# Kernel tuning notes

Hardware: AMD Instinct MI355X
Metric: run time of the kernel (lower is better)

The kernel has to match this reference:

```python
import jax, jax.numpy as jnp
import numpy as np

DIM, NUM_HEADS, N_POINTS = 256, 8, 4
N_Q, N_KV = 32768, 32768


def setup_inputs() -> dict:
    key = jax.random.key(0)
    ks = jax.random.split(key, 16)
    C, H, P = DIM, NUM_HEADS, N_POINTS
    s = 1.0 / np.sqrt(C)
    inp = {
        "query": jax.random.normal(ks[0], (N_Q, C), jnp.float32),
        "key": jax.random.normal(ks[1], (N_KV, C), jnp.float32),
        "value": jax.random.normal(ks[2], (N_KV, C), jnp.float32),
        # reference_points: Linear(C, 2*H*P)
        "Wr": jax.random.normal(ks[3], (C, 2 * H * P), jnp.float32) * s,
        "br": jnp.zeros((2 * H * P,), jnp.float32),
        # offset_attn: Linear(C, H*P*2)
        "Wo": jax.random.normal(ks[4], (C, H * P * 2), jnp.float32) * s,
        "bo": jnp.zeros((H * P * 2,), jnp.float32),
        # value_proj: Linear(C, C)
        "Wv": jax.random.normal(ks[5], (C, C), jnp.float32) * s,
        "bv": jnp.zeros((C,), jnp.float32),
        # output_proj: Linear(C, C)
        "Wout": jax.random.normal(ks[6], (C, C), jnp.float32) * s,
        "bout": jnp.zeros((C,), jnp.float32),
    }
    return inp


def reference(query, key, value, Wr, br, Wo, bo, Wv, bv, Wout, bout):
    N, C = query.shape
    M = value.shape[0]
    H, P = NUM_HEADS, N_POINTS
    Ch = C // H

    # sampling locations in [0,1] (ref) plus unconstrained offsets
    ref = jax.nn.sigmoid((query @ Wr + br).reshape(N, H, P, 2))
    off = (query @ Wo + bo).reshape(N, H, P, 2)
    loc = ref + off                              # [N,H,P,2]

    # 1-D bilinear interpolation along the token axis. The original's
    # 4-term (wx,wy) expression algebraically collapses to a pure lerp in x:
    # (1-wx)(1-wy)+ (1-wx)wy = (1-wx), wx(1-wy)+wx*wy = wx.
    x = loc[..., 0] * (M - 1)                    # [N,H,P]
    x0 = jnp.clip(jnp.floor(x).astype(jnp.int32), 0, M - 1)
    x1 = jnp.clip(x0 + 1, 0, M - 1)
    wx = (x - x0.astype(x.dtype))[..., None]     # [N,H,P,1]

    hidx = jnp.arange(H)[None, :, None]          # head-aligned gather index

    def sample(table):                           # table: [M,H,Ch]
        g0 = table[x0, hidx]                     # [N,H,P,Ch]
        g1 = table[x1, hidx]
        return (1.0 - wx) * g0 + wx * g1

    v = (value @ Wv + bv).reshape(M, H, Ch)      # value_proj, split heads
    sv = sample(v)                               # [N,H,P,Ch] sampled values

    # attention weights from query/key: sample per-head keys at the same
    # locations, dot with per-head queries, softmax over the P points
    k = key.reshape(M, H, Ch)
    sk = sample(k)                               # [N,H,P,Ch]
    q = query.reshape(N, H, Ch)
    scores = jnp.einsum("nhc,nhpc->nhp", q, sk) / jnp.sqrt(
        jnp.asarray(Ch, query.dtype)
    )
    attn = jax.nn.softmax(scores, axis=-1)       # [N,H,P]

    out = jnp.einsum("nhp,nhpc->nhc", attn, sv).reshape(N, C)
    return out @ Wout + bout
```

## Files before the change

### kernel.cpp

```cpp
#include <hip/hip_runtime.h>
#include <hip/hip_bf16.h>
#include <stdint.h>

#define NQ    32768
#define NKV   32768
#define CDIM  256
#define NHEADS 8
#define NPTS  4

using bf16x8 = __attribute__((ext_vector_type(8))) short;
using f32x4  = __attribute__((ext_vector_type(4))) float;
using u16x8  = __attribute__((ext_vector_type(8))) ushort;

static __device__ __forceinline__ ushort f2bf(float f) {
  uint32_t u = __float_as_uint(f);
  return (ushort)((u + 0x7FFFu + ((u >> 16) & 1u)) >> 16);
}
static __device__ __forceinline__ float bf2f(ushort h) {
  return __uint_as_float(((uint32_t)h) << 16);
}
static __device__ __forceinline__ void async16(const void* g, void* l) {
  __builtin_amdgcn_global_load_lds(
      (const __attribute__((address_space(1))) uint32_t*)g,
      (__attribute__((address_space(3))) uint32_t*)l, 16, 0, 0);
}
#define WAIT_VM(N) do { asm volatile("s_waitcnt vmcnt(" #N ")" ::: "memory"); \
                        __builtin_amdgcn_sched_barrier(0); } while (0)

__global__ __launch_bounds__(256) void transpose_w(const float* __restrict__ W,
                                                   ushort* __restrict__ WT) {
  int j = blockIdx.x, k = threadIdx.x;
  WT[j * 256 + k] = f2bf(W[k * 256 + j]);
}

__global__ __launch_bounds__(256) void gemm_mfma(
    const ushort* __restrict__ A, const ushort* __restrict__ BT,
    const float* __restrict__ bias, ushort* __restrict__ Cb,
    float* __restrict__ Cf, int out_bf16) {
  __shared__ ushort Alds[128 * 32];
  __shared__ ushort Blds[128 * 32];
  const int t = threadIdx.x;
  const int wave = t >> 6, lane = t & 63;
  const int mt = blockIdx.x >> 1, nt = blockIdx.x & 1;
  const int m0 = mt * 128, n0 = nt * 128;
  const int wr = wave >> 1, wc = wave & 1;
  const int r16 = lane & 15, kb = (lane >> 4) * 8;

  f32x4 acc[4][4] = {};

  for (int kt = 0; kt < 256; kt += 32) {
    __syncthreads();
#pragma unroll
    for (int it = 0; it < 2; ++it) {
      int c = it * 256 + t;
      int row = c >> 2, cc = c & 3;
      async16(A  + ((size_t)(m0 + row) * 256 + kt + cc * 8),
              Alds + (size_t)(it * 256 + wave * 64) * 8);
      async16(BT + ((size_t)(n0 + row) * 256 + kt + cc * 8),
              Blds + (size_t)(it * 256 + wave * 64) * 8);
    }
    __syncthreads();

    bf16x8 af[4], bfr[4];
#pragma unroll
    for (int m = 0; m < 4; ++m)
      af[m] = *(const bf16x8*)&Alds[(wr * 64 + m * 16 + r16) * 32 + kb];
#pragma unroll
    for (int n = 0; n < 4; ++n)
      bfr[n] = *(const bf16x8*)&Blds[(wc * 64 + n * 16 + r16) * 32 + kb];
#pragma unroll
    for (int m = 0; m < 4; ++m)
#pragma unroll
      for (int n = 0; n < 4; ++n)
        acc[m][n] = __builtin_amdgcn_mfma_f32_16x16x32_bf16(af[m], bfr[n],
                                                            acc[m][n], 0, 0, 0);
  }

  const int rg = lane >> 4;
#pragma unroll
  for (int m = 0; m < 4; ++m)
#pragma unroll
    for (int n = 0; n < 4; ++n) {
      int gc = n0 + wc * 64 + n * 16 + r16;
      float bb = bias[gc];
#pragma unroll
      for (int r = 0; r < 4; ++r) {
        int gr = m0 + wr * 64 + m * 16 + rg * 4 + r;
        float v = acc[m][n][r] + bb;
        if (out_bf16) Cb[(size_t)gr * 256 + gc] = f2bf(v);
        else          Cf[(size_t)gr * 256 + gc] = v;
      }
    }
}

__global__ __launch_bounds__(256) void gemm_mfma_fa(
    const float* __restrict__ Af, const ushort* __restrict__ BT,
    const float* __restrict__ bias, ushort* __restrict__ Cb) {
  __shared__ ushort Alds[128 * 32];
  __shared__ ushort Blds[128 * 32];
  const int t = threadIdx.x;
  const int wave = t >> 6, lane = t & 63;
  const int mt = blockIdx.x >> 1, nt = blockIdx.x & 1;
  const int m0 = mt * 128, n0 = nt * 128;
  const int wr = wave >> 1, wc = wave & 1;
  const int r16 = lane & 15, kb = (lane >> 4) * 8;

  f32x4 acc[4][4] = {};

  for (int kt = 0; kt < 256; kt += 32) {
    __syncthreads();
#pragma unroll
    for (int it = 0; it < 2; ++it) {
      int c = it * 256 + t;
      int row = c >> 2, cc = c & 3;
      async16(BT + ((size_t)(n0 + row) * 256 + kt + cc * 8),
              Blds + (size_t)(it * 256 + wave * 64) * 8);
    }
#pragma unroll
    for (int it = 0; it < 2; ++it) {
      int c = it * 256 + t;
      int row = c >> 2, cc = c & 3;
      const float* src = Af + (size_t)(m0 + row) * 256 + kt + cc * 8;
      f32x4 a = *(const f32x4*)src;
      f32x4 b = *(const f32x4*)(src + 4);
      u16x8 w;
#pragma unroll
      for (int e = 0; e < 4; ++e) { w[e] = f2bf(a[e]); w[4 + e] = f2bf(b[e]); }
      *(u16x8*)&Alds[(size_t)c * 8] = w;
    }
    __syncthreads();

    bf16x8 af[4], bfr[4];
#pragma unroll
    for (int m = 0; m < 4; ++m)
      af[m] = *(const bf16x8*)&Alds[(wr * 64 + m * 16 + r16) * 32 + kb];
#pragma unroll
    for (int n = 0; n < 4; ++n)
      bfr[n] = *(const bf16x8*)&Blds[(wc * 64 + n * 16 + r16) * 32 + kb];
#pragma unroll
    for (int m = 0; m < 4; ++m)
#pragma unroll
      for (int n = 0; n < 4; ++n)
        acc[m][n] = __builtin_amdgcn_mfma_f32_16x16x32_bf16(af[m], bfr[n],
                                                            acc[m][n], 0, 0, 0);
  }

  const int rg = lane >> 4;
#pragma unroll
  for (int m = 0; m < 4; ++m)
#pragma unroll
    for (int n = 0; n < 4; ++n) {
      int gc = n0 + wc * 64 + n * 16 + r16;
      float bb = bias[gc];
#pragma unroll
      for (int r = 0; r < 4; ++r) {
        int gr = m0 + wr * 64 + m * 16 + rg * 4 + r;
        Cb[(size_t)gr * 256 + gc] = f2bf(acc[m][n][r] + bb);
      }
    }
}

__global__ __launch_bounds__(256) void loc_gemm(const float* __restrict__ Q,
                                                const float* __restrict__ Wr,
                                                const float* __restrict__ Wo,
                                                float* __restrict__ locr) {
  __shared__ float AT[64][68];
  __shared__ float Bl[64][64];
  const int m0 = blockIdx.x * 64;
  const int t = threadIdx.x;
  const int tr = t >> 4, tc = t & 15;
  float acc[4][4] = {};

  for (int k0 = 0; k0 < 256; k0 += 64) {
    __syncthreads();
#pragma unroll
    for (int i = 0; i < 4; ++i) {
      int row = (t >> 4) + 16 * i;
      int kk = (t & 15) * 4;
      float4 v = *(const float4*)&Q[(size_t)(m0 + row) * 256 + k0 + kk];
      AT[kk + 0][row] = v.x; AT[kk + 1][row] = v.y;
      AT[kk + 2][row] = v.z; AT[kk + 3][row] = v.w;
    }
#pragma unroll
    for (int i = 0; i < 16; ++i) {
      int j = t & 63;
      int kk = (t >> 6) + 4 * i;
      float v = (j < 32) ? Wr[(size_t)(k0 + kk) * 64 + 2 * j]
                         : Wo[(size_t)(k0 + kk) * 64 + 2 * (j - 32)];
      Bl[kk][j] = v;
    }
    __syncthreads();
#pragma unroll 8
    for (int kk = 0; kk < 64; ++kk) {
      float4 a = *(const float4*)&AT[kk][tr * 4];
      float4 b = *(const float4*)&Bl[kk][tc * 4];
      float av[4] = {a.x, a.y, a.z, a.w};
      float bv4[4] = {b.x, b.y, b.z, b.w};
#pragma unroll
      for (int i = 0; i < 4; ++i)
#pragma unroll
        for (int jj = 0; jj < 4; ++jj) acc[i][jj] += av[i] * bv4[jj];
    }
  }
#pragma unroll
  for (int i = 0; i < 4; ++i)
#pragma unroll
    for (int jj = 0; jj < 4; ++jj)
      locr[(size_t)(m0 + tr * 4 + i) * 64 + tc * 4 + jj] = acc[i][jj];
}

__global__ __launch_bounds__(256) void sample_attn(
    const float* __restrict__ query, const float* __restrict__ key,
    const ushort* __restrict__ vtab, const float* __restrict__ locr,
    const float* __restrict__ br, const float* __restrict__ bo,
    ushort* __restrict__ out2) {
  __shared__ char smem[4][13312];
  const int wave = threadIdx.x >> 6, l = threadIdx.x & 63;
  const int j = l & 31;
  const int n = blockIdx.x * 4 + wave;
  const int Mm1 = NKV - 1;
  char* kbuf = smem[wave];
  char* vbuf = kbuf + 8192;
  char* qbuf = kbuf + 12288;

  float rr = locr[(size_t)n * 64 + j];
  float oo = locr[(size_t)n * 64 + 32 + j];
  float ref = 1.0f / (1.0f + expf(-(rr + br[2 * j])));
  float x = (ref + (oo + bo[2 * j])) * (float)Mm1;
  float xf = floorf(x);
  int x0 = (int)fminf(fmaxf(xf, 0.0f), (float)Mm1);
  int x1 = (x0 + 1 > Mm1) ? Mm1 : x0 + 1;
  float wx = x - (float)x0;
  float w0 = 1.0f - wx;

  {
    int hq = l >> 3, cq = l & 7;
    async16(query + (size_t)n * 256 + hq * 32 + ((cq ^ hq) << 2), qbuf);
  }
  {
    int ptg = l >> 3, s7 = l & 7;
    int kch = s7 ^ ptg;
#pragma unroll
    for (int i = 0; i < 8; ++i) {
      int pt = ((i & 3) << 3) + ptg;
      int row = (i < 4) ? __shfl(x0, pt, 64) : __shfl(x1, pt, 64);
      int hs = pt >> 2;
      async16(key + (size_t)row * 256 + hs * 32 + (kch << 2), kbuf + i * 1024);
    }
  }
  {
    int cg = (l & 3) ^ ((l >> 2) & 3) ^ ((l >> 4) & 3);
#pragma unroll
    for (int i = 0; i < 4; ++i) {
      int pt = ((i & 1) << 4) + (l >> 2);
      int row = (i < 2) ? __shfl(x0, pt, 64) : __shfl(x1, pt, 64);
      int hp = pt >> 2;
      async16(vtab + (size_t)row * 256 + hp * 32 + cg * 8, vbuf + i * 1024);
    }
  }

  WAIT_VM(4);

  float dot = 0.f;
  {
    int h = (l & 31) >> 2;
#pragma unroll
    for (int c = 0; c < 8; ++c) {
      f32x4 qc = *(const f32x4*)(qbuf + ((h << 3) + (c ^ h)) * 16);
      f32x4 kc = *(const f32x4*)(kbuf + l * 128 + ((c ^ (l & 7)) << 4));
#pragma unroll
      for (int e = 0; e < 4; ++e) dot += qc[e] * kc[e];
    }
  }
  float other = __shfl_xor(dot, 32, 64);
  float d0 = (l < 32) ? dot : other;
  float d1 = (l < 32) ? other : dot;
  float score = (w0 * d0 + wx * d1) * 0.17677669529663687f;

  float m1 = fmaxf(score, __shfl_xor(score, 1, 64));
  float mx = fmaxf(m1, __shfl_xor(m1, 2, 64));
  float e0 = expf(score - mx);
  float s1 = e0 + __shfl_xor(e0, 1, 64);
  float ssum = s1 + __shfl_xor(s1, 2, 64);
  float attn = e0 / ssum;
  float c0 = attn * w0, c1 = attn * wx;

  const int oh = l >> 3, os = l & 7;
  float cc0[4], cc1[4];
#pragma unroll
  for (int m = 0; m < 4; ++m) {
    cc0[m] = __shfl(c0, oh * 4 + m, 64);
    cc1[m] = __shfl(c1, oh * 4 + m, 64);
  }

  WAIT_VM(0);

  float acc[4] = {};
#pragma unroll
  for (int m = 0; m < 4; ++m) {
    int pt = oh * 4 + m;
    int slot = (os >> 1) ^ m ^ (oh & 3);
    int off = slot * 16 + (os & 1) * 8;
    ushort4 v0 = *(const ushort4*)(vbuf + pt * 64 + off);
    ushort4 v1 = *(const ushort4*)(vbuf + (pt + 32) * 64 + off);
#pragma unroll
    for (int e = 0; e < 4; ++e) {
      float ve0 = bf2f((&v0.x)[e]), ve1 = bf2f((&v1.x)[e]);
      acc[e] += cc0[m] * ve0 + cc1[m] * ve1;
    }
  }
  ushort4 ow;
#pragma unroll
  for (int e = 0; e < 4; ++e) (&ow.x)[e] = f2bf(acc[e]);
  *(ushort4*)(out2 + (size_t)n * 256 + oh * 32 + os * 4) = ow;
}

extern "C" void kernel_launch(void* const* d_in, const int* in_sizes, int n_in,
                              void* d_out, int out_size, void* d_ws, size_t ws_size,
                              hipStream_t stream) {
  const float* query = (const float*)d_in[0];
  const float* key   = (const float*)d_in[1];
  const float* value = (const float*)d_in[2];
  const float* Wr    = (const float*)d_in[3];
  const float* br    = (const float*)d_in[4];
  const float* Wo    = (const float*)d_in[5];
  const float* bo    = (const float*)d_in[6];
  const float* Wv    = (const float*)d_in[7];
  const float* bv    = (const float*)d_in[8];
  const float* Wout  = (const float*)d_in[9];
  const float* bout  = (const float*)d_in[10];
  float* out = (float*)d_out;

  char* ws = (char*)d_ws;
  ushort* out2  = (ushort*)(ws);
  ushort* vtab  = (ushort*)(ws + (16u << 20));
  float*  locr  = (float*) (ws + (32u << 20));
  ushort* WvT   = (ushort*)(ws + (40u << 20));
  ushort* WoT   = (ushort*)(ws + (40u << 20) + (1u << 17));

  transpose_w<<<256, 256, 0, stream>>>(Wv, WvT);
  transpose_w<<<256, 256, 0, stream>>>(Wout, WoT);
  gemm_mfma_fa<<<(NQ / 128) * 2, 256, 0, stream>>>(value, WvT, bv, vtab);
  loc_gemm<<<NQ / 64, 256, 0, stream>>>(query, Wr, Wo, locr);
  sample_attn<<<NQ / 4, 256, 0, stream>>>(query, key, vtab, locr, br, bo, out2);
  gemm_mfma<<<(NQ / 128) * 2, 256, 0, stream>>>(out2, WoT, bout, nullptr, out, 0);
}
```

Measured before the change: 102.3 us.

## Store value table head-major so one 128B load fetches both lerp rows

The value projection GEMM now writes its bf16 output head-major ([H][NKV][32]). Rows x0 and x0+1 of a head are then adjacent, so a single 128-byte region covers both interpolation taps, and the sampler issues half as many value gathers. The x0==M-1 edge case folds the second weight into the first. Query is loaded straight into registers instead of through LDS, and the key and value LDS swizzles are redone. The head-major store from the GEMM is strided and less coalesced, which may cost time in that kernel.

```diff
diff --git a/kernel.cpp b/kernel.cpp
--- a/kernel.cpp
+++ b/kernel.cpp
@@ -95,7 +95,7 @@
 
 __global__ __launch_bounds__(256) void gemm_mfma_fa(
     const float* __restrict__ Af, const ushort* __restrict__ BT,
-    const float* __restrict__ bias, ushort* __restrict__ Cb) {
+    const float* __restrict__ bias, ushort* __restrict__ CbT) {
   __shared__ ushort Alds[128 * 32];
   __shared__ ushort Blds[128 * 32];
   const int t = threadIdx.x;
@@ -155,7 +155,8 @@
 #pragma unroll
       for (int r = 0; r < 4; ++r) {
         int gr = m0 + wr * 64 + m * 16 + rg * 4 + r;
-        Cb[(size_t)gr * 256 + gc] = f2bf(acc[m][n][r] + bb);
+        CbT[((size_t)(gc >> 5) * NKV + gr) * 32 + (gc & 31)] =
+            f2bf(acc[m][n][r] + bb);
       }
     }
 }
@@ -211,17 +212,16 @@
 
 __global__ __launch_bounds__(256) void sample_attn(
     const float* __restrict__ query, const float* __restrict__ key,
-    const ushort* __restrict__ vtab, const float* __restrict__ locr,
+    const ushort* __restrict__ vtabT, const float* __restrict__ locr,
     const float* __restrict__ br, const float* __restrict__ bo,
     ushort* __restrict__ out2) {
-  __shared__ char smem[4][13312];
+  __shared__ char smem[4][12288];
   const int wave = threadIdx.x >> 6, l = threadIdx.x & 63;
   const int j = l & 31;
   const int n = blockIdx.x * 4 + wave;
   const int Mm1 = NKV - 1;
   char* kbuf = smem[wave];
   char* vbuf = kbuf + 8192;
-  char* qbuf = kbuf + 12288;
 
   float rr = locr[(size_t)n * 64 + j];
   float oo = locr[(size_t)n * 64 + 32 + j];
@@ -233,44 +233,46 @@
   float wx = x - (float)x0;
   float w0 = 1.0f - wx;
 
+  const float* qr = query + (size_t)n * 256 + (j >> 2) * 32;
+  f32x4 qv[8];
+#pragma unroll
+  for (int c = 0; c < 8; ++c) qv[c] = *(const f32x4*)(qr + c * 4);
+  __builtin_amdgcn_sched_barrier(0);
+
   {
-    int hq = l >> 3, cq = l & 7;
-    async16(query + (size_t)n * 256 + hq * 32 + ((cq ^ hq) << 2), qbuf);
-  }
-  {
-    int ptg = l >> 3, s7 = l & 7;
-    int kch = s7 ^ ptg;
+    const int ptg = l >> 3, p7 = l & 7;
 #pragma unroll
     for (int i = 0; i < 8; ++i) {
       int pt = ((i & 3) << 3) + ptg;
       int row = (i < 4) ? __shfl(x0, pt, 64) : __shfl(x1, pt, 64);
-      int hs = pt >> 2;
-      async16(key + (size_t)row * 256 + hs * 32 + (kch << 2), kbuf + i * 1024);
-    }
-  }
+      int sc = p7 ^ ptg ^ (i & 3);
+      async16(key + (size_t)row * 256 + (pt >> 2) * 32 + (sc << 2),
+              kbuf + i * 1024);
+    }
+  }
+  __builtin_amdgcn_sched_barrier(0);
   {
-    int cg = (l & 3) ^ ((l >> 2) & 3) ^ ((l >> 4) & 3);
+    const int pg3 = l >> 3, c7 = l & 7;
+    const int sc = c7 ^ pg3;
 #pragma unroll
     for (int i = 0; i < 4; ++i) {
-      int pt = ((i & 1) << 4) + (l >> 2);
-      int row = (i < 2) ? __shfl(x0, pt, 64) : __shfl(x1, pt, 64);
-      int hp = pt >> 2;
-      async16(vtab + (size_t)row * 256 + hp * 32 + cg * 8, vbuf + i * 1024);
-    }
-  }
+      int pg = i * 8 + pg3;
+      int row = __shfl(x0, pg, 64);
+      async16(vtabT + ((size_t)(pg >> 2) * NKV + row) * 32 + sc * 8,
+              vbuf + i * 1024);
+    }
+  }
+  __builtin_amdgcn_sched_barrier(0);
 
   WAIT_VM(4);
 
   float dot = 0.f;
-  {
-    int h = (l & 31) >> 2;
-#pragma unroll
-    for (int c = 0; c < 8; ++c) {
-      f32x4 qc = *(const f32x4*)(qbuf + ((h << 3) + (c ^ h)) * 16);
-      f32x4 kc = *(const f32x4*)(kbuf + l * 128 + ((c ^ (l & 7)) << 4));
-#pragma unroll
-      for (int e = 0; e < 4; ++e) dot += qc[e] * kc[e];
-    }
+#pragma unroll
+  for (int c = 0; c < 8; ++c) {
+    int pos = c ^ (l & 7) ^ ((l >> 3) & 3);
+    f32x4 kc = *(const f32x4*)(kbuf + l * 128 + pos * 16);
+#pragma unroll
+    for (int e = 0; e < 4; ++e) dot += qv[c][e] * kc[e];
   }
   float other = __shfl_xor(dot, 32, 64);
   float d0 = (l < 32) ? dot : other;
@@ -283,14 +285,16 @@
   float s1 = e0 + __shfl_xor(e0, 1, 64);
   float ssum = s1 + __shfl_xor(s1, 2, 64);
   float attn = e0 / ssum;
-  float c0 = attn * w0, c1 = attn * wx;
+  int edge = (x0 == Mm1);
+  float c1v = edge ? 0.0f : attn * wx;
+  float c0v = edge ? attn * (w0 + wx) : attn * w0;
 
   const int oh = l >> 3, os = l & 7;
   float cc0[4], cc1[4];
 #pragma unroll
   for (int m = 0; m < 4; ++m) {
-    cc0[m] = __shfl(c0, oh * 4 + m, 64);
-    cc1[m] = __shfl(c1, oh * 4 + m, 64);
+    cc0[m] = __shfl(c0v, oh * 4 + m, 64);
+    cc1[m] = __shfl(c1v, oh * 4 + m, 64);
   }
 
   WAIT_VM(0);
@@ -299,15 +303,14 @@
 #pragma unroll
   for (int m = 0; m < 4; ++m) {
     int pt = oh * 4 + m;
-    int slot = (os >> 1) ^ m ^ (oh & 3);
-    int off = slot * 16 + (os & 1) * 8;
-    ushort4 v0 = *(const ushort4*)(vbuf + pt * 64 + off);
-    ushort4 v1 = *(const ushort4*)(vbuf + (pt + 32) * 64 + off);
-#pragma unroll
-    for (int e = 0; e < 4; ++e) {
-      float ve0 = bf2f((&v0.x)[e]), ve1 = bf2f((&v1.x)[e]);
-      acc[e] += cc0[m] * ve0 + cc1[m] * ve1;
-    }
+    int pos0 = (os >> 1) ^ (pt & 7);
+    int pos1 = (4 + (os >> 1)) ^ (pt & 7);
+    const char* pb = vbuf + pt * 128 + (os & 1) * 8;
+    ushort4 v0 = *(const ushort4*)(pb + pos0 * 16);
+    ushort4 v1 = *(const ushort4*)(pb + pos1 * 16);
+#pragma unroll
+    for (int e = 0; e < 4; ++e)
+      acc[e] += cc0[m] * bf2f((&v0.x)[e]) + cc1[m] * bf2f((&v1.x)[e]);
   }
   ushort4 ow;
 #pragma unroll
@@ -333,15 +336,15 @@
 
   char* ws = (char*)d_ws;
   ushort* out2  = (ushort*)(ws);
-  ushort* vtab  = (ushort*)(ws + (16u << 20));
+  ushort* vtabT = (ushort*)(ws + (16u << 20));
   float*  locr  = (float*) (ws + (32u << 20));
   ushort* WvT   = (ushort*)(ws + (40u << 20));
   ushort* WoT   = (ushort*)(ws + (40u << 20) + (1u << 17));
 
   transpose_w<<<256, 256, 0, stream>>>(Wv, WvT);
   transpose_w<<<256, 256, 0, stream>>>(Wout, WoT);
-  gemm_mfma_fa<<<(NQ / 128) * 2, 256, 0, stream>>>(value, WvT, bv, vtab);
+  gemm_mfma_fa<<<(NQ / 128) * 2, 256, 0, stream>>>(value, WvT, bv, vtabT);
   loc_gemm<<<NQ / 64, 256, 0, stream>>>(query, Wr, Wo, locr);
-  sample_attn<<<NQ / 4, 256, 0, stream>>>(query, key, vtab, locr, br, bo, out2);
+  sample_attn<<<NQ / 4, 256, 0, stream>>>(query, key, vtabT, locr, br, bo, out2);
   gemm_mfma<<<(NQ / 128) * 2, 256, 0, stream>>>(out2, WoT, bout, nullptr, out, 0);
 }
```

After: 100.9 us. No clear change (-1.4%).
